# Optimization experiments

Hardware: AMD Instinct MI355X
Metric: run time of the kernel (lower is better)

The kernel has to match this reference:

```python
import jax, jax.numpy as jnp
from jax import lax
import numpy as np

AMP_MAX = 3.0
GATE_BIAS = float(np.log(0.65 / 0.35))  # sigmoid(GATE_BIAS) = gate_bias_init = 0.65


def setup_inputs() -> dict:
    key = jax.random.key(0)
    k0, k1, k2 = jax.random.split(key, 3)
    B, n, d, K = 4, 4096, 1024, 256
    x = jax.random.normal(k0, (B, n, d), jnp.float32)
    W_proj = jax.random.normal(k1, (4 * K, d), jnp.float32) * (1.0 / np.sqrt(d))
    b_proj = jnp.zeros((4 * K,), jnp.float32)
    W_res = jax.random.normal(k2, (d, K), jnp.float32) * 0.002  # nn.init.normal_(std=0.002)
    res_scale = jnp.asarray(0.05, jnp.float32)
    return {"x": x, "W_proj": W_proj, "b_proj": b_proj, "W_res": W_res, "res_scale": res_scale}


def _scan_combine(c1, c2):
    # first-order linear recurrence r_t = a_t * r_{t-1} + b_t (complex b as (br, bi))
    a1, br1, bi1 = c1
    a2, br2, bi2 = c2
    return (a1 * a2, a2 * br1 + br2, a2 * bi1 + bi2)


def reference(x, W_proj, b_proj, W_res, res_scale):
    B, n, d = x.shape
    K = W_res.shape[1]
    # OscillatorProjection: Linear(d_model -> 4K), chunk into A, omega, phi, alpha
    raw = jnp.einsum("bnd,kd->bnk", x, W_proj) + b_proj  # (B, n, 4K)
    a_raw, w_raw, p_raw, g_raw = jnp.split(raw, 4, axis=-1)
    A = AMP_MAX * jax.nn.sigmoid(a_raw)            # amplitude in (0, amplitude_max)
    omega = jax.nn.softplus(w_raw)                 # positive frequency
    phi = p_raw                                    # phase
    alpha = jax.nn.sigmoid(g_raw + GATE_BIAS)      # decay gate, init ~0.65

    positions = jnp.log1p(jnp.arange(n, dtype=jnp.float32))[None, :, None]  # phase_mode='log'
    angle = omega * positions + phi                # (B, n, K)
    cos_a = jnp.cos(angle)
    sin_a = jnp.sin(angle)
    one_m_a = 1.0 - alpha
    drive_r = one_m_a * A * cos_a
    drive_i = one_m_a * A * sin_a

    # O(log n) associative parallel scan over time
    _, r_r, r_i = lax.associative_scan(_scan_combine, (alpha, drive_r, drive_i), axis=1)

    # per-channel max-abs state norm: r /= max(max(|r_r|, |r_i|), 1.0)
    scale = jnp.maximum(jnp.maximum(jnp.abs(r_r), jnp.abs(r_i)), 1.0)
    r_r = r_r / scale
    r_i = r_i / scale

    # demodulate: Re(r * exp(-j*angle))
    rho = r_r * cos_a + r_i * sin_a                # (B, n, K)
    return res_scale * jnp.einsum("bnk,dk->bnd", rho, W_res)
```

## Files before the change

kernel.cpp:

```cpp
#include <hip/hip_runtime.h>
#include <stdint.h>

#define GATE_BIAS 0.6190392084062235f
#define N_TIME 4096
#define NCH 128
#define CHL 32

typedef __attribute__((ext_vector_type(4))) short sh4;
typedef __attribute__((ext_vector_type(8))) short sh8;
typedef __attribute__((ext_vector_type(4))) float f32x4;

__device__ __forceinline__ short f2bf(float f) {
  uint32_t u = __float_as_uint(f);
  u = (u + 0x7fffu + ((u >> 16) & 1u)) >> 16;
  return (short)u;
}
__device__ __forceinline__ float bf2f(short s) {
  return __uint_as_float(((uint32_t)(uint16_t)s) << 16);
}

__global__ __launch_bounds__(256) void k_gemm1(const float* __restrict__ x,
                                               const float* __restrict__ Wp,
                                               const float* __restrict__ bp,
                                               float* __restrict__ raw) {
  __shared__ short Ah[128][40], Al[128][40], Bh[128][40], Bl[128][40];
  const int t = threadIdx.x;
  const int row0 = blockIdx.x * 128;
  const int col0 = blockIdx.y * 128;
  const int lane = t & 63;
  const int wave = t >> 6;
  const int wm = wave >> 1, wn = wave & 1;
  const int lrow = lane & 15;
  const int lk = (lane >> 4) * 8;

  f32x4 acc[4][4];
#pragma unroll
  for (int i = 0; i < 4; ++i)
#pragma unroll
    for (int j = 0; j < 4; ++j) acc[i][j] = (f32x4)0.0f;

  for (int k0 = 0; k0 < 1024; k0 += 32) {
    __syncthreads();
#pragma unroll
    for (int i = 0; i < 4; ++i) {
      int f = t + 256 * i;
      int r = f >> 3, c4 = f & 7;
      float4 va = *(const float4*)(x  + (size_t)(row0 + r) * 1024 + k0 + c4 * 4);
      float4 vb = *(const float4*)(Wp + (size_t)(col0 + r) * 1024 + k0 + c4 * 4);
      sh4 ah, al, bh, bl;
      ah[0] = f2bf(va.x); al[0] = f2bf(va.x - bf2f(ah[0]));
      ah[1] = f2bf(va.y); al[1] = f2bf(va.y - bf2f(ah[1]));
      ah[2] = f2bf(va.z); al[2] = f2bf(va.z - bf2f(ah[2]));
      ah[3] = f2bf(va.w); al[3] = f2bf(va.w - bf2f(ah[3]));
      bh[0] = f2bf(vb.x); bl[0] = f2bf(vb.x - bf2f(bh[0]));
      bh[1] = f2bf(vb.y); bl[1] = f2bf(vb.y - bf2f(bh[1]));
      bh[2] = f2bf(vb.z); bl[2] = f2bf(vb.z - bf2f(bh[2]));
      bh[3] = f2bf(vb.w); bl[3] = f2bf(vb.w - bf2f(bh[3]));
      *(sh4*)&Ah[r][c4 * 4] = ah;
      *(sh4*)&Al[r][c4 * 4] = al;
      *(sh4*)&Bh[r][c4 * 4] = bh;
      *(sh4*)&Bl[r][c4 * 4] = bl;
    }
    __syncthreads();

    sh8 a_h[4], a_l[4], b_h[4], b_l[4];
#pragma unroll
    for (int mi = 0; mi < 4; ++mi) {
      a_h[mi] = *(const sh8*)&Ah[wm * 64 + mi * 16 + lrow][lk];
      a_l[mi] = *(const sh8*)&Al[wm * 64 + mi * 16 + lrow][lk];
      b_h[mi] = *(const sh8*)&Bh[wn * 64 + mi * 16 + lrow][lk];
      b_l[mi] = *(const sh8*)&Bl[wn * 64 + mi * 16 + lrow][lk];
    }
#pragma unroll
    for (int mi = 0; mi < 4; ++mi)
#pragma unroll
      for (int ni = 0; ni < 4; ++ni) {
        acc[mi][ni] = __builtin_amdgcn_mfma_f32_16x16x32_bf16(a_h[mi], b_h[ni], acc[mi][ni], 0, 0, 0);
        acc[mi][ni] = __builtin_amdgcn_mfma_f32_16x16x32_bf16(a_h[mi], b_l[ni], acc[mi][ni], 0, 0, 0);
        acc[mi][ni] = __builtin_amdgcn_mfma_f32_16x16x32_bf16(a_l[mi], b_h[ni], acc[mi][ni], 0, 0, 0);
      }
  }

#pragma unroll
  for (int ni = 0; ni < 4; ++ni) {
    int col = col0 + wn * 64 + ni * 16 + lrow;
    float bias = bp[col];
#pragma unroll
    for (int mi = 0; mi < 4; ++mi)
#pragma unroll
      for (int r = 0; r < 4; ++r) {
        int row = row0 + wm * 64 + mi * 16 + (lane >> 4) * 4 + r;
        raw[(size_t)row * 1024 + col] = acc[mi][ni][r] + bias;
      }
  }
}

__device__ __forceinline__ void activ(const float* __restrict__ rowp, int k, float pos,
                                      float& alpha, float& dr, float& di,
                                      float& cs, float& sn) {
  float a_raw = rowp[k];
  float w_raw = rowp[256 + k];
  float p_raw = rowp[512 + k];
  float g_raw = rowp[768 + k];
  alpha = 1.0f / (1.0f + __expf(-(g_raw + GATE_BIAS)));
  float A = 3.0f / (1.0f + __expf(-a_raw));
  float omega = (w_raw > 15.0f) ? w_raw : __logf(1.0f + __expf(w_raw));
  float angle = fmaf(omega, pos, p_raw);
  __sincosf(angle, &sn, &cs);
  float g = (1.0f - alpha) * A;
  dr = g * cs;
  di = g * sn;
}

__global__ __launch_bounds__(256) void k_scan1(const float* __restrict__ raw,
                                               float* __restrict__ totA,
                                               float* __restrict__ totR,
                                               float* __restrict__ totI) {
  const int k = threadIdx.x;
  const int c = blockIdx.x;
  const int b = blockIdx.y;
  const int t0 = c * CHL;
  float Aacc = 1.0f, rr = 0.0f, ri = 0.0f;
  for (int i = 0; i < CHL; ++i) {
    int t = t0 + i;
    const float* rowp = raw + (size_t)(b * N_TIME + t) * 1024;
    float pos = __logf((float)(t + 1));
    float alpha, dr, di, cs, sn;
    activ(rowp, k, pos, alpha, dr, di, cs, sn);
    rr = fmaf(alpha, rr, dr);
    ri = fmaf(alpha, ri, di);
    Aacc *= alpha;
  }
  int idx = (b * NCH + c) * 256 + k;
  totA[idx] = Aacc;
  totR[idx] = rr;
  totI[idx] = ri;
}

__global__ __launch_bounds__(256) void k_scan2(const float* __restrict__ totA,
                                               const float* __restrict__ totR,
                                               const float* __restrict__ totI,
                                               float* __restrict__ carR,
                                               float* __restrict__ carI) {
  const int k = threadIdx.x;
  const int b = blockIdx.x;
  float rr = 0.0f, ri = 0.0f;
  for (int c = 0; c < NCH; ++c) {
    int idx = (b * NCH + c) * 256 + k;
    carR[idx] = rr;
    carI[idx] = ri;
    float A = totA[idx];
    rr = fmaf(A, rr, totR[idx]);
    ri = fmaf(A, ri, totI[idx]);
  }
}

__global__ __launch_bounds__(256) void k_scan3(float* __restrict__ raw,
                                               const float* __restrict__ carR,
                                               const float* __restrict__ carI) {
  const int k = threadIdx.x;
  const int c = blockIdx.x;
  const int b = blockIdx.y;
  const int t0 = c * CHL;
  int idx = (b * NCH + c) * 256 + k;
  float rr = carR[idx];
  float ri = carI[idx];
  for (int i = 0; i < CHL; ++i) {
    int t = t0 + i;
    float* rowp = raw + (size_t)(b * N_TIME + t) * 1024;
    float pos = __logf((float)(t + 1));
    float alpha, dr, di, cs, sn;
    activ(rowp, k, pos, alpha, dr, di, cs, sn);
    rr = fmaf(alpha, rr, dr);
    ri = fmaf(alpha, ri, di);
    float scale = fmaxf(fmaxf(fabsf(rr), fabsf(ri)), 1.0f);
    float rho = (rr * cs + ri * sn) / scale;
    rowp[k] = rho;
  }
}

__global__ __launch_bounds__(256) void k_gemm2(const float* __restrict__ rho,
                                               const float* __restrict__ Wr,
                                               const float* __restrict__ rs_ptr,
                                               float* __restrict__ out) {
  __shared__ short Ah[128][40], Bh[128][40];
  const int t = threadIdx.x;
  const int row0 = blockIdx.x * 128;
  const int col0 = blockIdx.y * 128;
  const int lane = t & 63;
  const int wave = t >> 6;
  const int wm = wave >> 1, wn = wave & 1;
  const int lrow = lane & 15;
  const int lk = (lane >> 4) * 8;
  const float rs = *rs_ptr;

  f32x4 acc[4][4];
#pragma unroll
  for (int i = 0; i < 4; ++i)
#pragma unroll
    for (int j = 0; j < 4; ++j) acc[i][j] = (f32x4)0.0f;

  for (int k0 = 0; k0 < 256; k0 += 32) {
    __syncthreads();
#pragma unroll
    for (int i = 0; i < 4; ++i) {
      int f = t + 256 * i;
      int r = f >> 3, c4 = f & 7;
      float4 va = *(const float4*)(rho + (size_t)(row0 + r) * 1024 + k0 + c4 * 4);
      float4 vb = *(const float4*)(Wr  + (size_t)(col0 + r) * 256  + k0 + c4 * 4);
      sh4 ah, bh;
      ah[0] = f2bf(va.x); ah[1] = f2bf(va.y); ah[2] = f2bf(va.z); ah[3] = f2bf(va.w);
      bh[0] = f2bf(vb.x); bh[1] = f2bf(vb.y); bh[2] = f2bf(vb.z); bh[3] = f2bf(vb.w);
      *(sh4*)&Ah[r][c4 * 4] = ah;
      *(sh4*)&Bh[r][c4 * 4] = bh;
    }
    __syncthreads();

    sh8 a_f[4], b_f[4];
#pragma unroll
    for (int mi = 0; mi < 4; ++mi) {
      a_f[mi] = *(const sh8*)&Ah[wm * 64 + mi * 16 + lrow][lk];
      b_f[mi] = *(const sh8*)&Bh[wn * 64 + mi * 16 + lrow][lk];
    }
#pragma unroll
    for (int mi = 0; mi < 4; ++mi)
#pragma unroll
      for (int ni = 0; ni < 4; ++ni)
        acc[mi][ni] = __builtin_amdgcn_mfma_f32_16x16x32_bf16(a_f[mi], b_f[ni], acc[mi][ni], 0, 0, 0);
  }

#pragma unroll
  for (int ni = 0; ni < 4; ++ni) {
    int col = col0 + wn * 64 + ni * 16 + lrow;
#pragma unroll
    for (int mi = 0; mi < 4; ++mi)
#pragma unroll
      for (int r = 0; r < 4; ++r) {
        int row = row0 + wm * 64 + mi * 16 + (lane >> 4) * 4 + r;
        out[(size_t)row * 1024 + col] = rs * acc[mi][ni][r];
      }
  }
}

extern "C" void kernel_launch(void* const* d_in, const int* in_sizes, int n_in,
                              void* d_out, int out_size, void* d_ws, size_t ws_size,
                              hipStream_t stream) {
  const float* x  = (const float*)d_in[0];
  const float* Wp = (const float*)d_in[1];
  const float* bp = (const float*)d_in[2];
  const float* Wr = (const float*)d_in[3];
  const float* rs = (const float*)d_in[4];
  float* out = (float*)d_out;

  float* raw  = (float*)d_ws;
  float* totA = raw + (size_t)16384 * 1024;
  float* totR = totA + 4 * NCH * 256;
  float* totI = totR + 4 * NCH * 256;
  float* carR = totI + 4 * NCH * 256;
  float* carI = carR + 4 * NCH * 256;

  k_gemm1<<<dim3(128, 8), 256, 0, stream>>>(x, Wp, bp, raw);
  k_scan1<<<dim3(NCH, 4), 256, 0, stream>>>(raw, totA, totR, totI);
  k_scan2<<<4, 256, 0, stream>>>(totA, totR, totI, carR, carI);
  k_scan3<<<dim3(NCH, 4), 256, 0, stream>>>(raw, carR, carI);
  k_gemm2<<<dim3(128, 8), 256, 0, stream>>>(raw, Wr, rs, out);
}
```

Measured before the change: 331.0 us.

## Pre-split weights to bf16 hi/lo and store rho as compact bf16

Adds small pre-pass kernels that convert W_proj into bf16 hi/lo halves and W_res into bf16 once per call. gemm1 then loads the weight tiles directly instead of re-splitting them in every tile, which cuts its conversion ALU work and global reads. scan3 now writes rho as bf16 into a dense 256-wide buffer rather than fp32 into the 1024-wide raw buffer, so gemm2 reads far fewer bytes. The cost is two extra kernel launches and additional workspace.

```diff
diff --git a/kernel.cpp b/kernel.cpp
--- a/kernel.cpp
+++ b/kernel.cpp
@@ -19,8 +19,37 @@
   return __uint_as_float(((uint32_t)(uint16_t)s) << 16);
 }
 
+__global__ __launch_bounds__(256) void k_split(const float* __restrict__ src,
+                                               short* __restrict__ dh,
+                                               short* __restrict__ dl, int n4) {
+  int i = blockIdx.x * 256 + threadIdx.x;
+  int stride = gridDim.x * 256;
+  for (; i < n4; i += stride) {
+    float4 v = *(const float4*)(src + (size_t)i * 4);
+    sh4 h, l;
+    h[0] = f2bf(v.x); l[0] = f2bf(v.x - bf2f(h[0]));
+    h[1] = f2bf(v.y); l[1] = f2bf(v.y - bf2f(h[1]));
+    h[2] = f2bf(v.z); l[2] = f2bf(v.z - bf2f(h[2]));
+    h[3] = f2bf(v.w); l[3] = f2bf(v.w - bf2f(h[3]));
+    *(sh4*)(dh + (size_t)i * 4) = h;
+    *(sh4*)(dl + (size_t)i * 4) = l;
+  }
+}
+__global__ __launch_bounds__(256) void k_cvt(const float* __restrict__ src,
+                                             short* __restrict__ dst, int n4) {
+  int i = blockIdx.x * 256 + threadIdx.x;
+  int stride = gridDim.x * 256;
+  for (; i < n4; i += stride) {
+    float4 v = *(const float4*)(src + (size_t)i * 4);
+    sh4 h;
+    h[0] = f2bf(v.x); h[1] = f2bf(v.y); h[2] = f2bf(v.z); h[3] = f2bf(v.w);
+    *(sh4*)(dst + (size_t)i * 4) = h;
+  }
+}
+
 __global__ __launch_bounds__(256) void k_gemm1(const float* __restrict__ x,
-                                               const float* __restrict__ Wp,
+                                               const short* __restrict__ wph,
+                                               const short* __restrict__ wpl,
                                                const float* __restrict__ bp,
                                                float* __restrict__ raw) {
   __shared__ short Ah[128][40], Al[128][40], Bh[128][40], Bl[128][40];
@@ -45,21 +74,22 @@
     for (int i = 0; i < 4; ++i) {
       int f = t + 256 * i;
       int r = f >> 3, c4 = f & 7;
-      float4 va = *(const float4*)(x  + (size_t)(row0 + r) * 1024 + k0 + c4 * 4);
-      float4 vb = *(const float4*)(Wp + (size_t)(col0 + r) * 1024 + k0 + c4 * 4);
-      sh4 ah, al, bh, bl;
+      float4 va = *(const float4*)(x + (size_t)(row0 + r) * 1024 + k0 + c4 * 4);
+      sh4 ah, al;
       ah[0] = f2bf(va.x); al[0] = f2bf(va.x - bf2f(ah[0]));
       ah[1] = f2bf(va.y); al[1] = f2bf(va.y - bf2f(ah[1]));
       ah[2] = f2bf(va.z); al[2] = f2bf(va.z - bf2f(ah[2]));
       ah[3] = f2bf(va.w); al[3] = f2bf(va.w - bf2f(ah[3]));
-      bh[0] = f2bf(vb.x); bl[0] = f2bf(vb.x - bf2f(bh[0]));
-      bh[1] = f2bf(vb.y); bl[1] = f2bf(vb.y - bf2f(bh[1]));
-      bh[2] = f2bf(vb.z); bl[2] = f2bf(vb.z - bf2f(bh[2]));
-      bh[3] = f2bf(vb.w); bl[3] = f2bf(vb.w - bf2f(bh[3]));
       *(sh4*)&Ah[r][c4 * 4] = ah;
       *(sh4*)&Al[r][c4 * 4] = al;
-      *(sh4*)&Bh[r][c4 * 4] = bh;
-      *(sh4*)&Bl[r][c4 * 4] = bl;
+    }
+#pragma unroll
+    for (int i = 0; i < 2; ++i) {
+      int f = t + 256 * i;
+      int r = f >> 2, c8 = f & 3;
+      size_t g = (size_t)(col0 + r) * 1024 + k0 + c8 * 8;
+      *(sh8*)&Bh[r][c8 * 8] = *(const sh8*)(wph + g);
+      *(sh8*)&Bl[r][c8 * 8] = *(const sh8*)(wpl + g);
     }
     __syncthreads();
 
@@ -145,6 +175,7 @@
   const int k = threadIdx.x;
   const int b = blockIdx.x;
   float rr = 0.0f, ri = 0.0f;
+#pragma unroll 8
   for (int c = 0; c < NCH; ++c) {
     int idx = (b * NCH + c) * 256 + k;
     carR[idx] = rr;
@@ -155,9 +186,10 @@
   }
 }
 
-__global__ __launch_bounds__(256) void k_scan3(float* __restrict__ raw,
+__global__ __launch_bounds__(256) void k_scan3(const float* __restrict__ raw,
                                                const float* __restrict__ carR,
-                                               const float* __restrict__ carI) {
+                                               const float* __restrict__ carI,
+                                               short* __restrict__ rho_b) {
   const int k = threadIdx.x;
   const int c = blockIdx.x;
   const int b = blockIdx.y;
@@ -167,7 +199,7 @@
   float ri = carI[idx];
   for (int i = 0; i < CHL; ++i) {
     int t = t0 + i;
-    float* rowp = raw + (size_t)(b * N_TIME + t) * 1024;
+    const float* rowp = raw + (size_t)(b * N_TIME + t) * 1024;
     float pos = __logf((float)(t + 1));
     float alpha, dr, di, cs, sn;
     activ(rowp, k, pos, alpha, dr, di, cs, sn);
@@ -175,12 +207,12 @@
     ri = fmaf(alpha, ri, di);
     float scale = fmaxf(fmaxf(fabsf(rr), fabsf(ri)), 1.0f);
     float rho = (rr * cs + ri * sn) / scale;
-    rowp[k] = rho;
-  }
-}
-
-__global__ __launch_bounds__(256) void k_gemm2(const float* __restrict__ rho,
-                                               const float* __restrict__ Wr,
+    rho_b[(size_t)(b * N_TIME + t) * 256 + k] = f2bf(rho);
+  }
+}
+
+__global__ __launch_bounds__(256) void k_gemm2(const short* __restrict__ rho_b,
+                                               const short* __restrict__ wrb,
                                                const float* __restrict__ rs_ptr,
                                                float* __restrict__ out) {
   __shared__ short Ah[128][40], Bh[128][40];
@@ -203,16 +235,11 @@
   for (int k0 = 0; k0 < 256; k0 += 32) {
     __syncthreads();
 #pragma unroll
-    for (int i = 0; i < 4; ++i) {
+    for (int i = 0; i < 2; ++i) {
       int f = t + 256 * i;
-      int r = f >> 3, c4 = f & 7;
-      float4 va = *(const float4*)(rho + (size_t)(row0 + r) * 1024 + k0 + c4 * 4);
-      float4 vb = *(const float4*)(Wr  + (size_t)(col0 + r) * 256  + k0 + c4 * 4);
-      sh4 ah, bh;
-      ah[0] = f2bf(va.x); ah[1] = f2bf(va.y); ah[2] = f2bf(va.z); ah[3] = f2bf(va.w);
-      bh[0] = f2bf(vb.x); bh[1] = f2bf(vb.y); bh[2] = f2bf(vb.z); bh[3] = f2bf(vb.w);
-      *(sh4*)&Ah[r][c4 * 4] = ah;
-      *(sh4*)&Bh[r][c4 * 4] = bh;
+      int r = f >> 2, c8 = f & 3;
+      *(sh8*)&Ah[r][c8 * 8] = *(const sh8*)(rho_b + (size_t)(row0 + r) * 256 + k0 + c8 * 8);
+      *(sh8*)&Bh[r][c8 * 8] = *(const sh8*)(wrb  + (size_t)(col0 + r) * 256 + k0 + c8 * 8);
     }
     __syncthreads();
 
@@ -252,16 +279,24 @@
   const float* rs = (const float*)d_in[4];
   float* out = (float*)d_out;
 
-  float* raw  = (float*)d_ws;
-  float* totA = raw + (size_t)16384 * 1024;
-  float* totR = totA + 4 * NCH * 256;
-  float* totI = totR + 4 * NCH * 256;
-  float* carR = totI + 4 * NCH * 256;
-  float* carI = carR + 4 * NCH * 256;
-
-  k_gemm1<<<dim3(128, 8), 256, 0, stream>>>(x, Wp, bp, raw);
+  char* base = (char*)d_ws;
+  float* raw   = (float*)base;
+  float* totA  = (float*)(base + 67108864);
+  float* totR  = totA + 131072;
+  float* totI  = totR + 131072;
+  float* carR  = totI + 131072;
+  float* carI  = carR + 131072;
+  short* wph   = (short*)(base + 69730304);
+  short* wpl   = (short*)(base + 71827456);
+  short* wrb   = (short*)(base + 73924608);
+  short* rho_b = (short*)(base + 74448896);
+
+  k_split<<<1024, 256, 0, stream>>>(Wp, wph, wpl, 262144);
+  k_cvt  <<<256,  256, 0, stream>>>(Wr, wrb, 65536);
+
+  k_gemm1<<<dim3(128, 8), 256, 0, stream>>>(x, wph, wpl, bp, raw);
   k_scan1<<<dim3(NCH, 4), 256, 0, stream>>>(raw, totA, totR, totI);
   k_scan2<<<4, 256, 0, stream>>>(totA, totR, totI, carR, carI);
-  k_scan3<<<dim3(NCH, 4), 256, 0, stream>>>(raw, carR, carI);
-  k_gemm2<<<dim3(128, 8), 256, 0, stream>>>(raw, Wr, rs, out);
-}
+  k_scan3<<<dim3(NCH, 4), 256, 0, stream>>>(raw, carR, carI, rho_b);
+  k_gemm2<<<dim3(128, 8), 256, 0, stream>>>(rho_b, wrb, rs, out);
+}
```

Measured after the change: 298.7 us. -9.7%, faster.
